# Kernel optimization log

Measured on AMD Instinct MI355X. Metric: run time of the kernel, lower is better.

Reference implementation:

```python
import jax, jax.numpy as jnp
import numpy as np

N_NODES = 50000
N_GRAPHS = 512

def _glorot(key, shape):
    fan_in, fan_out = shape[1], shape[0]
    lim = np.sqrt(6.0 / (fan_in + fan_out))
    return jax.random.uniform(key, shape, jnp.float32, -lim, lim)

def setup_inputs() -> dict:
    key = jax.random.key(0)
    ks = jax.random.split(key, 12)
    x = jax.random.normal(ks[0], (N_NODES, 128), jnp.float32)
    edge_index = jax.random.randint(ks[1], (2, 800000), 0, N_NODES, jnp.int64)
    batch = jnp.sort(jax.random.randint(ks[2], (N_NODES,), 0, N_GRAPHS, jnp.int64))
    return {
        "x": x,
        "edge_index": edge_index,
        "batch": batch,
        "W1": _glorot(ks[3], (256, 128)), "b1": jnp.zeros((256,), jnp.float32),
        "W2": _glorot(ks[4], (256, 256)), "b2": jnp.zeros((256,), jnp.float32),
        "W3": _glorot(ks[5], (256, 256)), "b3": jnp.zeros((256,), jnp.float32),
        "Wf1": _glorot(ks[6], (128, 256)), "bf1": jnp.zeros((128,), jnp.float32),
        "Wf2": _glorot(ks[7], (10, 128)), "bf2": jnp.zeros((10,), jnp.float32),
    }

def _gin_conv(h, edge_index, W, b):
    # GINConv (eps=0): lin(x_i + sum_{j in N(i)} x_j)
    src, dst = edge_index[0], edge_index[1]
    aggr = jax.ops.segment_sum(h[src], dst, num_segments=N_NODES)
    return (h + aggr) @ W.T + b

def reference(x, edge_index, batch, W1, b1, W2, b2, W3, b3, Wf1, bf1, Wf2, bf2):
    h = jax.nn.relu(_gin_conv(x, edge_index, W1, b1))
    h = jax.nn.relu(_gin_conv(h, edge_index, W2, b2))
    h = jax.nn.relu(_gin_conv(h, edge_index, W3, b3))
    # global mean pool over graphs
    sums = jax.ops.segment_sum(h, batch, num_segments=N_GRAPHS)
    counts = jax.ops.segment_sum(jnp.ones((N_NODES,), h.dtype), batch, num_segments=N_GRAPHS)
    hg = sums / jnp.maximum(counts, 1.0)[:, None]
    h = jax.nn.relu(hg @ Wf1.T + bf1)
    return h @ Wf2.T + bf2
```

## Files before the change

### kernel.cpp

```cpp
#include <hip/hip_runtime.h>

#define N_NODES 50000
#define N_GRAPHS 512
#define N_EDGES 800000
#define NBKT 49

typedef __attribute__((ext_vector_type(8))) short short8;
typedef __attribute__((ext_vector_type(8))) unsigned short ushort8;
typedef __attribute__((ext_vector_type(4))) float floatx4;
typedef __attribute__((ext_vector_type(2))) float floatx2;

__device__ __forceinline__ float bf2f(unsigned short u) {
    union { unsigned int i; float f; } c;
    c.i = ((unsigned int)u) << 16;
    return c.f;
}
__device__ __forceinline__ unsigned short f2bf(float f) {
    union { float f; unsigned int i; } c;
    c.f = f;
    unsigned int u = c.i;
    return (unsigned short)((u + 0x7fffu + ((u >> 16) & 1u)) >> 16);
}

__device__ __forceinline__ unsigned char ftofp8(float f) {
    union { float f; unsigned int u; } c; c.f = f;
    unsigned int s = (c.u >> 24) & 0x80u;
    float a = fabsf(f);
    if (a < 0x1p-6f) return (unsigned char)s;
    if (a > 448.f)   return (unsigned char)(s | 0x7E);
    unsigned int u = c.u & 0x7FFFFFFFu;
    unsigned int r = u + 0x7FFFFu + ((u >> 20) & 1u);
    return (unsigned char)(s | (((r >> 23) - 120u) << 3) | ((r >> 20) & 7u));
}

__device__ __forceinline__ void f8acc(float* acc, uint2 v) {
    floatx2 a = __builtin_amdgcn_cvt_pk_f32_fp8(v.x, false);
    floatx2 b = __builtin_amdgcn_cvt_pk_f32_fp8(v.x, true);
    floatx2 c = __builtin_amdgcn_cvt_pk_f32_fp8(v.y, false);
    floatx2 d = __builtin_amdgcn_cvt_pk_f32_fp8(v.y, true);
    acc[0] += a[0]; acc[1] += a[1]; acc[2] += b[0]; acc[3] += b[1];
    acc[4] += c[0]; acc[5] += c[1]; acc[6] += d[0]; acc[7] += d[1];
}

__device__ __forceinline__ void g2lds16(const unsigned short* g, void* lds) {
    __builtin_amdgcn_global_load_lds(
        (const __attribute__((address_space(1))) void*)g,
        (__attribute__((address_space(3))) void*)lds, 16, 0, 0);
}

__global__ void conv_deg(const float* __restrict__ x, const float* __restrict__ W1,
                         const float* __restrict__ W2, const float* __restrict__ W3,
                         const int* __restrict__ dst,
                         unsigned char* __restrict__ xf8, unsigned short* __restrict__ o1,
                         unsigned short* __restrict__ o2, unsigned short* __restrict__ o3,
                         int* __restrict__ deg, float4* __restrict__ sums4) {
    int i = blockIdx.x * blockDim.x + threadIdx.x;
    if (i >= 2440960) {
        int j = i - 2440960;
        if (j < 32768) sums4[j] = make_float4(0.f, 0.f, 0.f, 0.f);
        return;
    }
    if (i >= 1640960) {
        int e = i - 1640960;
        atomicAdd(&deg[dst[e]], 1);
        return;
    }
    if (i < 1600000) {
        float4 v = ((const float4*)x)[i];
        uchar4 o;
        o.x = ftofp8(v.x); o.y = ftofp8(v.y); o.z = ftofp8(v.z); o.w = ftofp8(v.w);
        ((uchar4*)xf8)[i] = o;
        return;
    }
    int j = i - 1600000;
    const float* src; unsigned short* out; int base;
    if (j < 8192)       { src = W1; out = o1; base = j; }
    else if (j < 24576) { src = W2; out = o2; base = j - 8192; }
    else                { src = W3; out = o3; base = j - 24576; }
    float4 v = ((const float4*)src)[base];
    ushort4 o;
    o.x = f2bf(v.x); o.y = f2bf(v.y); o.z = f2bf(v.z); o.w = f2bf(v.w);
    ((ushort4*)out)[base] = o;
}

__global__ __launch_bounds__(1024) void scan1(const int* __restrict__ deg,
                                              int* __restrict__ rowptr,
                                              int* __restrict__ blocksum) {
    __shared__ int s[1024];
    int t = threadIdx.x;
    int i = blockIdx.x * 1024 + t;
    int v = (i < N_NODES) ? deg[i] : 0;
    s[t] = v;
    __syncthreads();
    for (int off = 1; off < 1024; off <<= 1) {
        int add = (t >= off) ? s[t - off] : 0;
        __syncthreads();
        s[t] += add;
        __syncthreads();
    }
    if (i < N_NODES) rowptr[i] = s[t] - v;
    if (t == 1023) blocksum[blockIdx.x] = s[t];
}

__global__ __launch_bounds__(1024) void scan3(int* __restrict__ rowptr,
                                              const int* __restrict__ blocksum,
                                              int* __restrict__ cursor,
                                              int* __restrict__ gcursor) {
    __shared__ int bse[64];
    int t = threadIdx.x;
    if (t < 64) {
        const int NB = (N_NODES + 1023) / 1024;
        int orig = (t < NB) ? blocksum[t] : 0;
        int v = orig;
        for (int off = 1; off < 64; off <<= 1) {
            int u = __shfl_up(v, off, 64);
            if (t >= off) v += u;
        }
        bse[t] = v - orig;
    }
    __syncthreads();
    int i = blockIdx.x * 1024 + t;
    if (i < N_NODES) {
        int v = rowptr[i] + bse[i >> 10];
        rowptr[i] = v;
        cursor[i] = v;
        if ((i & 1023) == 0) gcursor[i >> 10] = v;
    }
    if (i == 0) rowptr[N_NODES] = N_EDGES;
}

__global__ __launch_bounds__(256) void bin_edges(const int* __restrict__ src,
                                                 const int* __restrict__ dst,
                                                 int* __restrict__ gcursor,
                                                 unsigned int* __restrict__ staging) {
    __shared__ int cnt[NBKT];
    __shared__ int base[NBKT];
    int t = threadIdx.x;
    if (t < NBKT) cnt[t] = 0;
    __syncthreads();
    int e0 = blockIdx.x * 2048;
    int d[8], s[8];
#pragma unroll
    for (int r = 0; r < 8; r++) {
        int e = e0 + r * 256 + t;
        if (e < N_EDGES) {
            d[r] = dst[e]; s[r] = src[e];
            atomicAdd(&cnt[d[r] >> 10], 1);
        } else d[r] = -1;
    }
    __syncthreads();
    if (t < NBKT) base[t] = atomicAdd(&gcursor[t], cnt[t]);
    __syncthreads();
#pragma unroll
    for (int r = 0; r < 8; r++) {
        if (d[r] >= 0) {
            int off = atomicAdd(&base[d[r] >> 10], 1);
            staging[off] = ((unsigned)d[r] << 16) | (unsigned)s[r];
        }
    }
}

__global__ __launch_bounds__(1024) void scatter_bkt(const unsigned int* __restrict__ staging,
                                                    const int* __restrict__ rowptr,
                                                    int* __restrict__ cursor,
                                                    unsigned short* __restrict__ csr) {
    int b = blockIdx.x;
    int lo = rowptr[b << 10];
    int nhi = (b + 1) << 10; if (nhi > N_NODES) nhi = N_NODES;
    int hi = rowptr[nhi];
    for (int p = lo + threadIdx.x; p < hi; p += 1024) {
        unsigned v = staging[p];
        int d = v >> 16;
        int pos = atomicAdd(&cursor[d], 1);
        csr[pos] = (unsigned short)(v & 0xFFFFu);
    }
}

template <int C>
__global__ __launch_bounds__(256) void gather_f8(const unsigned char* __restrict__ h,
                                                 const int* __restrict__ rowptr,
                                                 const unsigned short* __restrict__ csr,
                                                 unsigned short* __restrict__ agg) {
    const int TPN = C / 8;
    const int NPB = 256 / TPN;
    int t = threadIdx.x;
    int n = blockIdx.x * NPB + t / TPN;
    if (n >= N_NODES) return;
    int c8 = t % TPN;
    const uint2* hp = (const uint2*)h + c8;
    float acc[8];
#pragma unroll
    for (int j = 0; j < 8; j++) acc[j] = 0.f;
    f8acc(acc, hp[(size_t)n * TPN]);
    int p = rowptr[n], end = rowptr[n + 1];
    for (; p + 8 <= end; p += 8) {
        int j0 = csr[p],     j1 = csr[p + 1], j2 = csr[p + 2], j3 = csr[p + 3];
        int j4 = csr[p + 4], j5 = csr[p + 5], j6 = csr[p + 6], j7 = csr[p + 7];
        uint2 v0 = hp[(size_t)j0 * TPN];
        uint2 v1 = hp[(size_t)j1 * TPN];
        uint2 v2 = hp[(size_t)j2 * TPN];
        uint2 v3 = hp[(size_t)j3 * TPN];
        uint2 v4 = hp[(size_t)j4 * TPN];
        uint2 v5 = hp[(size_t)j5 * TPN];
        uint2 v6 = hp[(size_t)j6 * TPN];
        uint2 v7 = hp[(size_t)j7 * TPN];
        f8acc(acc, v0); f8acc(acc, v1); f8acc(acc, v2); f8acc(acc, v3);
        f8acc(acc, v4); f8acc(acc, v5); f8acc(acc, v6); f8acc(acc, v7);
    }
    for (; p + 4 <= end; p += 4) {
        int j0 = csr[p], j1 = csr[p + 1], j2 = csr[p + 2], j3 = csr[p + 3];
        uint2 v0 = hp[(size_t)j0 * TPN];
        uint2 v1 = hp[(size_t)j1 * TPN];
        uint2 v2 = hp[(size_t)j2 * TPN];
        uint2 v3 = hp[(size_t)j3 * TPN];
        f8acc(acc, v0); f8acc(acc, v1); f8acc(acc, v2); f8acc(acc, v3);
    }
    for (; p < end; ++p) {
        uint2 v = hp[(size_t)csr[p] * TPN];
        f8acc(acc, v);
    }
    ushort8 o;
#pragma unroll
    for (int j = 0; j < 8; j++) o[j] = f2bf(acc[j]);
    ((ushort8*)agg)[(size_t)n * TPN + c8] = o;
}

template <int K, int F8OUT>
__global__ __launch_bounds__(256) void gemm_mfma64(
    const unsigned short* __restrict__ A, const unsigned short* __restrict__ W,
    const float* __restrict__ bias, void* __restrict__ Cout, int M) {
    __shared__ short8 As[256];
    __shared__ short8 Ws[512];

    int tid = threadIdx.x;
    int wave = tid >> 6, lane = tid & 63;
    int wm = wave & 1, wn = wave >> 1;
    int rowbase = blockIdx.x * 64;
    int colbase = blockIdx.y * 128;
    int lkc = lane >> 4, lr = lane & 15;
    int rsw = lr ^ (lkc << 2);
    int rslot = lkc * 16 + rsw;

    int ar = rowbase + wave * 16 + rsw; if (ar >= M) ar = M - 1;
    int wr0 = colbase + (0 * 4 + wave) * 16 + rsw;
    int wr1 = colbase + (1 * 4 + wave) * 16 + rsw;
    char* asb  = (char*)As + (size_t)(wave * 64) * 16;
    char* wsb0 = (char*)Ws + (size_t)(0 * 256 + wave * 64) * 16;
    char* wsb1 = (char*)Ws + (size_t)(1 * 256 + wave * 64) * 16;

    floatx4 acc[2][4];
#pragma unroll
    for (int i = 0; i < 2; i++)
#pragma unroll
        for (int j = 0; j < 4; j++) acc[i][j] = (floatx4)(0.f);

#pragma unroll 2
    for (int k0 = 0; k0 < K; k0 += 32) {
        int ks = k0 + lkc * 8;
        g2lds16(A + (size_t)ar * K + ks, asb);
        g2lds16(W + (size_t)wr0 * K + ks, wsb0);
        g2lds16(W + (size_t)wr1 * K + ks, wsb1);
        __syncthreads();

        short8 af[2], wf[4];
#pragma unroll
        for (int mt = 0; mt < 2; mt++) af[mt] = As[(wm * 2 + mt) * 64 + rslot];
#pragma unroll
        for (int nt = 0; nt < 4; nt++) wf[nt] = Ws[(wn * 4 + nt) * 64 + rslot];
#pragma unroll
        for (int mt = 0; mt < 2; mt++)
#pragma unroll
            for (int nt = 0; nt < 4; nt++)
                acc[mt][nt] = __builtin_amdgcn_mfma_f32_16x16x32_bf16(
                    af[mt], wf[nt], acc[mt][nt], 0, 0, 0);
        __syncthreads();
    }

#pragma unroll
    for (int mt = 0; mt < 2; mt++) {
#pragma unroll
        for (int reg = 0; reg < 4; reg++) {
            int row = rowbase + (wm * 2 + mt) * 16 + lkc * 4 + reg;
            if (row >= M) continue;
#pragma unroll
            for (int nt = 0; nt < 4; nt++) {
                int col = colbase + (wn * 4 + nt) * 16 + lr;
                float v = fmaxf(acc[mt][nt][reg] + bias[col], 0.f);
                if (F8OUT)
                    ((unsigned char*)Cout)[(size_t)row * 256 + col] = ftofp8(v);
                else
                    ((unsigned short*)Cout)[(size_t)row * 256 + col] = f2bf(v);
            }
        }
    }
}

__global__ __launch_bounds__(256) void pool_accum(const unsigned short* __restrict__ h,
                                                  const int* __restrict__ batch,
                                                  float* __restrict__ sums) {
    int t = threadIdx.x;
    int r0 = blockIdx.x * 32;
    int r1 = r0 + 32; if (r1 > N_NODES) r1 = N_NODES;
    if (r0 >= N_NODES) return;
    float acc = 0.f;
    int gcur = batch[r0];
    for (int r = r0; r < r1; ++r) {
        int g = batch[r];
        if (g != gcur) { atomicAdd(&sums[gcur * 256 + t], acc); acc = 0.f; gcur = g; }
        acc += bf2f(h[(size_t)r * 256 + t]);
    }
    atomicAdd(&sums[gcur * 256 + t], acc);
}

__global__ __launch_bounds__(128) void head(const float* __restrict__ sums,
                                            const int* __restrict__ batch,
                                            const float* __restrict__ Wf1,
                                            const float* __restrict__ bf1,
                                            const float* __restrict__ Wf2,
                                            const float* __restrict__ bf2,
                                            float* __restrict__ out) {
    __shared__ float hg[256];
    __shared__ float hid[128];
    int g = blockIdx.x;
    int t = threadIdx.x;
    int lo = 0, hi = N_NODES;
    while (lo < hi) { int m = (lo + hi) >> 1; if (batch[m] < g) lo = m + 1; else hi = m; }
    int start = lo;
    lo = 0; hi = N_NODES;
    while (lo < hi) { int m = (lo + hi) >> 1; if (batch[m] < g + 1) lo = m + 1; else hi = m; }
    int end = lo;
    float inv = 1.0f / fmaxf((float)(end - start), 1.0f);
    hg[t]       = sums[g * 256 + t] * inv;
    hg[t + 128] = sums[g * 256 + t + 128] * inv;
    __syncthreads();
    float a1 = bf1[t];
    for (int c = 0; c < 256; c++) a1 += hg[c] * Wf1[t * 256 + c];
    hid[t] = fmaxf(a1, 0.f);
    __syncthreads();
    if (t < 10) {
        float a = bf2[t];
        for (int j = 0; j < 128; j++) a += hid[j] * Wf2[t * 128 + j];
        out[g * 10 + t] = a;
    }
}

extern "C" void kernel_launch(void* const* d_in, const int* in_sizes, int n_in,
                              void* d_out, int out_size, void* d_ws, size_t ws_size,
                              hipStream_t stream) {
    const float* x   = (const float*)d_in[0];
    const int*  edge = (const int*)d_in[1];
    const int*  batch= (const int*)d_in[2];
    const float* W1  = (const float*)d_in[3];
    const float* b1  = (const float*)d_in[4];
    const float* W2  = (const float*)d_in[5];
    const float* b2  = (const float*)d_in[6];
    const float* W3  = (const float*)d_in[7];
    const float* b3  = (const float*)d_in[8];
    const float* Wf1 = (const float*)d_in[9];
    const float* bf1 = (const float*)d_in[10];
    const float* Wf2 = (const float*)d_in[11];
    const float* bf2 = (const float*)d_in[12];
    const int* src = edge;
    const int* dst = edge + N_EDGES;

    char* wsb = (char*)d_ws;
    size_t off = 0;
    auto alloc = [&](size_t bytes) { void* p = wsb + off; off += (bytes + 255) & ~(size_t)255; return p; };
    unsigned char*  x_f8   = (unsigned char*)alloc((size_t)N_NODES * 128);
    unsigned char*  h1_f8  = (unsigned char*)alloc((size_t)N_NODES * 256);
    unsigned char*  h2_f8  = (unsigned char*)alloc((size_t)N_NODES * 256);
    unsigned short* agg_bf = (unsigned short*)alloc((size_t)N_NODES * 256 * 2);
    unsigned short* hA_bf  = (unsigned short*)alloc((size_t)N_NODES * 256 * 2);
    unsigned short* W1bf   = (unsigned short*)alloc(256 * 128 * 2);
    unsigned short* W2bf   = (unsigned short*)alloc(256 * 256 * 2);
    unsigned short* W3bf   = (unsigned short*)alloc(256 * 256 * 2);
    int* rowptr    = (int*)alloc((N_NODES + 4) * 4);
    int* cursor    = (int*)alloc(N_NODES * 4);
    int* deg       = (int*)alloc(N_NODES * 4);
    unsigned short* csr = (unsigned short*)alloc((size_t)N_EDGES * 2);
    unsigned int* staging = (unsigned int*)alloc((size_t)N_EDGES * 4);
    int* blocksum  = (int*)alloc(64 * 4);
    int* gcursor   = (int*)alloc(64 * 4);
    float* sums    = (float*)alloc((size_t)N_GRAPHS * 256 * 4);

    const int NB_SCAN = (N_NODES + 1023) / 1024;

    hipMemsetAsync(deg, 0, N_NODES * sizeof(int), stream);
    conv_deg<<<(2473728 + 255) / 256, 256, 0, stream>>>(
        x, W1, W2, W3, dst, x_f8, W1bf, W2bf, W3bf, deg, (float4*)sums);

    scan1<<<NB_SCAN, 1024, 0, stream>>>(deg, rowptr, blocksum);
    scan3<<<NB_SCAN, 1024, 0, stream>>>(rowptr, blocksum, cursor, gcursor);
    bin_edges<<<(N_EDGES + 2047) / 2048, 256, 0, stream>>>(src, dst, gcursor, staging);
    scatter_bkt<<<NBKT, 1024, 0, stream>>>(staging, rowptr, cursor, csr);

    dim3 ggrid((N_NODES + 63) / 64, 2);

    gather_f8<128><<<(N_NODES + 15) / 16, 256, 0, stream>>>(x_f8, rowptr, csr, agg_bf);
    gemm_mfma64<128, 1><<<ggrid, 256, 0, stream>>>(agg_bf, W1bf, b1, h1_f8, N_NODES);

    gather_f8<256><<<(N_NODES + 7) / 8, 256, 0, stream>>>(h1_f8, rowptr, csr, agg_bf);
    gemm_mfma64<256, 1><<<ggrid, 256, 0, stream>>>(agg_bf, W2bf, b2, h2_f8, N_NODES);

    gather_f8<256><<<(N_NODES + 7) / 8, 256, 0, stream>>>(h2_f8, rowptr, csr, agg_bf);
    gemm_mfma64<256, 0><<<ggrid, 256, 0, stream>>>(agg_bf, W3bf, b3, hA_bf, N_NODES);

    pool_accum<<<(N_NODES + 31) / 32, 256, 0, stream>>>(hA_bf, batch, sums);
    head<<<N_GRAPHS, 128, 0, stream>>>(sums, batch, Wf1, bf1, Wf2, bf2, (float*)d_out);
}
```

Before: 384.2 us.

## Build CSR via fixed-capacity buckets with per-bucket local histogram and scan

Replaces the global degree histogram, two-pass scan, and global cursor scatter with a bucketed build. Edges are binned into fixed-capacity buckets of 1024 destination nodes. Each bucket block then computes its own degree histogram, scan and CSR placement using shared-memory atomics. This drops the memset, the global atomic degree pass, and two scan kernels, at the cost of a larger staging buffer. It also assumes no bucket exceeds 20480 edges, which holds only for roughly uniform destination distributions.

```diff
diff --git a/kernel.cpp b/kernel.cpp
--- a/kernel.cpp
+++ b/kernel.cpp
@@ -4,6 +4,7 @@
 #define N_GRAPHS 512
 #define N_EDGES 800000
 #define NBKT 49
+#define BKT_CAP 20480
 
 typedef __attribute__((ext_vector_type(8))) short short8;
 typedef __attribute__((ext_vector_type(8))) unsigned short ushort8;
@@ -48,21 +49,16 @@
         (__attribute__((address_space(3))) void*)lds, 16, 0, 0);
 }
 
-__global__ void conv_deg(const float* __restrict__ x, const float* __restrict__ W1,
+__global__ void conv_all(const float* __restrict__ x, const float* __restrict__ W1,
                          const float* __restrict__ W2, const float* __restrict__ W3,
-                         const int* __restrict__ dst,
                          unsigned char* __restrict__ xf8, unsigned short* __restrict__ o1,
                          unsigned short* __restrict__ o2, unsigned short* __restrict__ o3,
-                         int* __restrict__ deg, float4* __restrict__ sums4) {
+                         float4* __restrict__ sums4, int* __restrict__ bktcnt) {
     int i = blockIdx.x * blockDim.x + threadIdx.x;
-    if (i >= 2440960) {
-        int j = i - 2440960;
+    if (i >= 1640960) {
+        int j = i - 1640960;
         if (j < 32768) sums4[j] = make_float4(0.f, 0.f, 0.f, 0.f);
-        return;
-    }
-    if (i >= 1640960) {
-        int e = i - 1640960;
-        atomicAdd(&deg[dst[e]], 1);
+        else if (j < 32832) bktcnt[j - 32768] = 0;
         return;
     }
     if (i < 1600000) {
@@ -83,34 +79,48 @@
     ((ushort4*)out)[base] = o;
 }
 
-__global__ __launch_bounds__(1024) void scan1(const int* __restrict__ deg,
-                                              int* __restrict__ rowptr,
-                                              int* __restrict__ blocksum) {
+__global__ __launch_bounds__(256) void bin_edges(const int* __restrict__ src,
+                                                 const int* __restrict__ dst,
+                                                 int* __restrict__ bktcnt,
+                                                 unsigned int* __restrict__ staging) {
+    __shared__ int cnt[NBKT];
+    __shared__ int base[NBKT];
+    int t = threadIdx.x;
+    if (t < NBKT) cnt[t] = 0;
+    __syncthreads();
+    int e0 = blockIdx.x * 2048;
+    int d[8], s[8];
+#pragma unroll
+    for (int r = 0; r < 8; r++) {
+        int e = e0 + r * 256 + t;
+        if (e < N_EDGES) {
+            d[r] = dst[e]; s[r] = src[e];
+            atomicAdd(&cnt[d[r] >> 10], 1);
+        } else d[r] = -1;
+    }
+    __syncthreads();
+    if (t < NBKT) base[t] = cnt[t] ? atomicAdd(&bktcnt[t], cnt[t]) : 0;
+    __syncthreads();
+#pragma unroll
+    for (int r = 0; r < 8; r++) {
+        if (d[r] >= 0) {
+            int bkt = d[r] >> 10;
+            int off = atomicAdd(&base[bkt], 1);
+            staging[(size_t)bkt * BKT_CAP + off] = ((unsigned)d[r] << 16) | (unsigned)s[r];
+        }
+    }
+}
+
+__global__ __launch_bounds__(1024) void bucket_build(
+    const unsigned int* __restrict__ staging, const int* __restrict__ bktcnt,
+    int* __restrict__ rowptr, unsigned short* __restrict__ csr) {
+    __shared__ int hist[1024];
     __shared__ int s[1024];
-    int t = threadIdx.x;
-    int i = blockIdx.x * 1024 + t;
-    int v = (i < N_NODES) ? deg[i] : 0;
-    s[t] = v;
-    __syncthreads();
-    for (int off = 1; off < 1024; off <<= 1) {
-        int add = (t >= off) ? s[t - off] : 0;
-        __syncthreads();
-        s[t] += add;
-        __syncthreads();
-    }
-    if (i < N_NODES) rowptr[i] = s[t] - v;
-    if (t == 1023) blocksum[blockIdx.x] = s[t];
-}
-
-__global__ __launch_bounds__(1024) void scan3(int* __restrict__ rowptr,
-                                              const int* __restrict__ blocksum,
-                                              int* __restrict__ cursor,
-                                              int* __restrict__ gcursor) {
     __shared__ int bse[64];
-    int t = threadIdx.x;
+    __shared__ int lcur[1024];
+    int b = blockIdx.x, t = threadIdx.x;
     if (t < 64) {
-        const int NB = (N_NODES + 1023) / 1024;
-        int orig = (t < NB) ? blocksum[t] : 0;
+        int orig = (t < NBKT) ? bktcnt[t] : 0;
         int v = orig;
         for (int off = 1; off < 64; off <<= 1) {
             int u = __shfl_up(v, off, 64);
@@ -118,61 +128,35 @@
         }
         bse[t] = v - orig;
     }
-    __syncthreads();
-    int i = blockIdx.x * 1024 + t;
-    if (i < N_NODES) {
-        int v = rowptr[i] + bse[i >> 10];
-        rowptr[i] = v;
-        cursor[i] = v;
-        if ((i & 1023) == 0) gcursor[i >> 10] = v;
-    }
-    if (i == 0) rowptr[N_NODES] = N_EDGES;
-}
-
-__global__ __launch_bounds__(256) void bin_edges(const int* __restrict__ src,
-                                                 const int* __restrict__ dst,
-                                                 int* __restrict__ gcursor,
-                                                 unsigned int* __restrict__ staging) {
-    __shared__ int cnt[NBKT];
-    __shared__ int base[NBKT];
-    int t = threadIdx.x;
-    if (t < NBKT) cnt[t] = 0;
-    __syncthreads();
-    int e0 = blockIdx.x * 2048;
-    int d[8], s[8];
-#pragma unroll
-    for (int r = 0; r < 8; r++) {
-        int e = e0 + r * 256 + t;
-        if (e < N_EDGES) {
-            d[r] = dst[e]; s[r] = src[e];
-            atomicAdd(&cnt[d[r] >> 10], 1);
-        } else d[r] = -1;
-    }
-    __syncthreads();
-    if (t < NBKT) base[t] = atomicAdd(&gcursor[t], cnt[t]);
-    __syncthreads();
-#pragma unroll
-    for (int r = 0; r < 8; r++) {
-        if (d[r] >= 0) {
-            int off = atomicAdd(&base[d[r] >> 10], 1);
-            staging[off] = ((unsigned)d[r] << 16) | (unsigned)s[r];
-        }
-    }
-}
-
-__global__ __launch_bounds__(1024) void scatter_bkt(const unsigned int* __restrict__ staging,
-                                                    const int* __restrict__ rowptr,
-                                                    int* __restrict__ cursor,
-                                                    unsigned short* __restrict__ csr) {
-    int b = blockIdx.x;
-    int lo = rowptr[b << 10];
-    int nhi = (b + 1) << 10; if (nhi > N_NODES) nhi = N_NODES;
-    int hi = rowptr[nhi];
-    for (int p = lo + threadIdx.x; p < hi; p += 1024) {
-        unsigned v = staging[p];
-        int d = v >> 16;
-        int pos = atomicAdd(&cursor[d], 1);
-        csr[pos] = (unsigned short)(v & 0xFFFFu);
+    hist[t] = 0;
+    __syncthreads();
+    int base = bse[b];
+    int cnt = bktcnt[b];
+    int n0 = b << 10;
+    const unsigned int* stg = staging + (size_t)b * BKT_CAP;
+    for (int p = t; p < cnt; p += 1024)
+        atomicAdd(&hist[(stg[p] >> 16) - n0], 1);
+    __syncthreads();
+    int v = hist[t];
+    s[t] = v;
+    __syncthreads();
+    for (int off = 1; off < 1024; off <<= 1) {
+        int add = (t >= off) ? s[t - off] : 0;
+        __syncthreads();
+        s[t] += add;
+        __syncthreads();
+    }
+    int excl = s[t] - v;
+    int node = n0 + t;
+    if (node < N_NODES) rowptr[node] = base + excl;
+    lcur[t] = base + excl;
+    if (b == NBKT - 1 && t == 0) rowptr[N_NODES] = N_EDGES;
+    __syncthreads();
+    for (int p = t; p < cnt; p += 1024) {
+        unsigned e = stg[p];
+        int li = (int)(e >> 16) - n0;
+        int pos = atomicAdd(&lcur[li], 1);
+        csr[pos] = (unsigned short)(e & 0xFFFFu);
     }
 }
 
@@ -375,24 +359,16 @@
     unsigned short* W2bf   = (unsigned short*)alloc(256 * 256 * 2);
     unsigned short* W3bf   = (unsigned short*)alloc(256 * 256 * 2);
     int* rowptr    = (int*)alloc((N_NODES + 4) * 4);
-    int* cursor    = (int*)alloc(N_NODES * 4);
-    int* deg       = (int*)alloc(N_NODES * 4);
     unsigned short* csr = (unsigned short*)alloc((size_t)N_EDGES * 2);
-    unsigned int* staging = (unsigned int*)alloc((size_t)N_EDGES * 4);
-    int* blocksum  = (int*)alloc(64 * 4);
-    int* gcursor   = (int*)alloc(64 * 4);
+    unsigned int* staging = (unsigned int*)alloc((size_t)NBKT * BKT_CAP * 4);
+    int* bktcnt    = (int*)alloc(64 * 4);
     float* sums    = (float*)alloc((size_t)N_GRAPHS * 256 * 4);
 
-    const int NB_SCAN = (N_NODES + 1023) / 1024;
-
-    hipMemsetAsync(deg, 0, N_NODES * sizeof(int), stream);
-    conv_deg<<<(2473728 + 255) / 256, 256, 0, stream>>>(
-        x, W1, W2, W3, dst, x_f8, W1bf, W2bf, W3bf, deg, (float4*)sums);
-
-    scan1<<<NB_SCAN, 1024, 0, stream>>>(deg, rowptr, blocksum);
-    scan3<<<NB_SCAN, 1024, 0, stream>>>(rowptr, blocksum, cursor, gcursor);
-    bin_edges<<<(N_EDGES + 2047) / 2048, 256, 0, stream>>>(src, dst, gcursor, staging);
-    scatter_bkt<<<NBKT, 1024, 0, stream>>>(staging, rowptr, cursor, csr);
+    conv_all<<<(1673792 + 255) / 256, 256, 0, stream>>>(
+        x, W1, W2, W3, x_f8, W1bf, W2bf, W3bf, (float4*)sums, bktcnt);
+
+    bin_edges<<<(N_EDGES + 2047) / 2048, 256, 0, stream>>>(src, dst, bktcnt, staging);
+    bucket_build<<<NBKT, 1024, 0, stream>>>(staging, bktcnt, rowptr, csr);
 
     dim3 ggrid((N_NODES + 63) / 64, 2);
 
```

Result: faster. 319.7 us (-16.8%).
